# Kernel tuning notes

Measured on AMD Instinct MI355X. Metric: run time of the kernel, lower is better.

## Reference

```python
import jax, jax.numpy as jnp
import numpy as np

SEQ_LEN = 256
E = 1024      # embedding_dim (= decoder LSTM hidden size)
H = 2048      # encoder hidden_dim
LAT = 512     # latent_space_dim
CLS = 512     # common_latent_space_dim
MIX = 384     # mixture_size
VJ = 64       # embedding_dim_VJ  (constraint: 2*VJ + LAT + MIX == E)
ALPH = 32; NVG = 64; NJG = 16
X_IDX = 0; B_IDX = 1  # indices of 'X' (start) and 'B' (stop) letters


def _lstm_final(xs, h0, c0, Wih, Whh, bih, bhh):
    """Run an LSTM over xs [T, B, in] and return the final hidden state [B, H]."""
    def step(carry, x):
        h, c = carry
        g = x @ Wih.T + bih + h @ Whh.T + bhh
        i, f, gg, o = jnp.split(g, 4, axis=-1)
        c = jax.nn.sigmoid(f) * c + jax.nn.sigmoid(i) * jnp.tanh(gg)
        h = jax.nn.sigmoid(o) * jnp.tanh(c)
        return (h, c), None
    (h, c), _ = jax.lax.scan(step, (h0, c0), xs)
    return h


def _decode(h0c, Wih, Whh, bih, bhh, start_vec, end_vec, n_steps):
    """Autoregressive LSTM decode: feed previous output back as next input.
    h0c [1,E] is used as both initial h and c (as in the source)."""
    def step(carry, _):
        h, c, prev = carry
        g = prev @ Wih.T + bih + h @ Whh.T + bhh
        i, f, gg, o = jnp.split(g, 4, axis=-1)
        c2 = jax.nn.sigmoid(f) * c + jax.nn.sigmoid(i) * jnp.tanh(gg)
        h2 = jax.nn.sigmoid(o) * jnp.tanh(c2)
        return (h2, c2, h2), h2
    _, ys = jax.lax.scan(step, (h0c, h0c, start_vec), None, length=n_steps)  # [T-2,1,E]
    seq = jnp.concatenate([start_vec[None], ys, end_vec[None]], axis=0)      # [T,1,E]
    return seq[::-1]  # source reverses the list before cat


def setup_inputs() -> dict:
    key = jax.random.key(0)
    ks = jax.random.split(key, 26)
    def g(k, shape):
        return jax.random.normal(k, shape, dtype=jnp.float32) * 0.05
    return {
        "x": jax.random.randint(ks[0], (SEQ_LEN,), 0, ALPH),
        "Vg": jax.random.randint(ks[1], (1,), 0, NVG),
        "Jg": jax.random.randint(ks[2], (1,), 0, NJG),
        "emb": g(ks[3], (ALPH, E)),
        "emb_Vg": g(ks[4], (NVG, VJ)),
        "emb_Jg": g(ks[5], (NJG, VJ)),
        "enc_Wih": g(ks[6], (4 * H, E)),
        "enc_Whh": g(ks[7], (4 * H, H)),
        "enc_bih": g(ks[8], (4 * H,)),
        "enc_bhh": g(ks[9], (4 * H,)),
        "cls_W": g(ks[10], (CLS, 2 * H)), "cls_b": g(ks[11], (CLS,)),
        "latf_W": g(ks[12], (LAT, H)), "latf_b": g(ks[13], (LAT,)),
        "latr_W": g(ks[14], (LAT, H)), "latr_b": g(ks[15], (LAT,)),
        "mix_W": g(ks[16], (MIX, CLS)), "mix_b": g(ks[17], (MIX,)),
        "recf_Wih": g(ks[18], (4 * E, E)), "recf_Whh": g(ks[19], (4 * E, E)),
        "recf_bih": g(ks[20], (4 * E,)), "recf_bhh": g(ks[21], (4 * E,)),
        "recr_Wih": g(ks[22], (4 * E, E)), "recr_Whh": g(ks[23], (4 * E, E)),
        "recr_bih": g(ks[24], (4 * E,)), "recr_bhh": g(ks[25], (4 * E,)),
    }


def reference(x, Vg, Jg, emb, emb_Vg, emb_Jg,
              enc_Wih, enc_Whh, enc_bih, enc_bhh,
              cls_W, cls_b, latf_W, latf_b, latr_W, latr_b,
              mix_W, mix_b,
              recf_Wih, recf_Whh, recf_bih, recf_bhh,
              recr_Wih, recr_Whh, recr_bih, recr_bhh):
    T = x.shape[0]
    emb_f = emb[x]          # [T, E]
    emb_r = emb_f[::-1]     # reversed sequence
    h0 = jnp.zeros((1, H), jnp.float32)
    # NB: the source (bug preserved) runs the reverse pass through lstm_in_f as well.
    hf = _lstm_final(emb_f[:, None, :], h0, h0, enc_Wih, enc_Whh, enc_bih, enc_bhh)  # [1,H]
    hr = _lstm_final(emb_r[:, None, :], h0, h0, enc_Wih, enc_Whh, enc_bih, enc_bhh)  # [1,H]
    # dropout treated in eval mode (identity) for a deterministic reference
    common = jnp.tanh(jnp.concatenate([hf, hr], axis=-1) @ cls_W.T + cls_b)  # [1,CLS]
    lat_f = hf @ latf_W.T + latf_b  # [1,LAT]
    lat_r = hr @ latr_W.T + latr_b
    vg = emb_Vg[Vg]  # [1,VJ]
    jg = emb_Jg[Jg]
    lat_f_full = jnp.concatenate([vg, lat_f, jg], axis=-1)  # [1, 2*VJ+LAT]
    lat_r_full = jnp.concatenate([vg, lat_r, jg], axis=-1)
    # source (bug preserved): mixture_to_f applied to both branches
    mix = common @ mix_W.T + mix_b                      # [1,MIX]
    h0f = jnp.concatenate([lat_f_full, mix], axis=-1)   # [1,E]
    h0r = jnp.concatenate([lat_r_full, mix], axis=-1)
    start = emb[X_IDX][None]  # 'X' embedding, [1,E]
    stop = emb[B_IDX][None]   # 'B' embedding
    rec_f = _decode(h0f, recf_Wih, recf_Whh, recf_bih, recf_bhh, start, stop, T - 2)
    rec_r = _decode(h0r, recr_Wih, recr_Whh, recr_bih, recr_bhh, stop, start, T - 2)
    return (lat_f_full[None], lat_r_full[None], rec_f, rec_r, emb_f, emb_r)
```

## Files before the change

### kernel.cpp

```cpp
#include <hip/hip_runtime.h>
#include <hip/hip_fp16.h>

#define NB 256
#define NT 512


struct KArgs {
  const int *x, *Vg, *Jg;
  const float *emb, *embVg, *embJg;
  const float *encWih, *encWhh, *encBih, *encBhh;
  const float *clsW, *clsB, *latfW, *latfB, *latrW, *latrB, *mixW, *mixB;
  const float *recWih[2], *recWhh[2], *recBih[2], *recBhh[2];
  float* out;
  unsigned* barFull;
  unsigned long long *eDat, *hTdec;
  float *common, *bsum, *d1, *embf, *P;
  int fast;
};

__device__ __forceinline__ unsigned long long packtag(unsigned tag, float f) {
  return ((unsigned long long)tag << 32) | (unsigned long long)__float_as_uint(f);
}
__device__ __forceinline__ float sigm(float x) { return 1.f / (1.f + __expf(-x)); }
__device__ __forceinline__ float tanh_(float x) { return 2.f / (1.f + __expf(-2.f * x)) - 1.f; }
__device__ __forceinline__ float wred(float v) {
#pragma unroll
  for (int off = 32; off; off >>= 1) v += __shfl_xor(v, off, 64);
  return v;
}
__device__ __forceinline__ void cstoref(float* p, float v) {
  __hip_atomic_store(p, v, __ATOMIC_RELAXED, __HIP_MEMORY_SCOPE_AGENT);
}
__device__ __forceinline__ float cloadf(const float* p) {
  return __hip_atomic_load(p, __ATOMIC_RELAXED, __HIP_MEMORY_SCOPE_AGENT);
}
__device__ __forceinline__ unsigned long long cload64(const unsigned long long* p) {
  return __hip_atomic_load(p, __ATOMIC_RELAXED, __HIP_MEMORY_SCOPE_AGENT);
}
__device__ __forceinline__ void cstore64(unsigned long long* p, unsigned long long v) {
  __hip_atomic_store(p, v, __ATOMIC_RELAXED, __HIP_MEMORY_SCOPE_AGENT);
}

__device__ __forceinline__ void gbar_tree(unsigned* tree, int idx, unsigned e) {
  const int ls = 8;
  __syncthreads();
  if (threadIdx.x == 0) {
    unsigned* leaf = tree + (idx >> 3) * ls;
    unsigned* root = tree + 32 * ls;
    unsigned* flag = root + ls;
    unsigned old = __hip_atomic_fetch_add(leaf, 1u, __ATOMIC_ACQ_REL, __HIP_MEMORY_SCOPE_AGENT);
    if (old == e * 8u - 1u) {
      unsigned ro = __hip_atomic_fetch_add(root, 1u, __ATOMIC_ACQ_REL, __HIP_MEMORY_SCOPE_AGENT);
      if (ro == e * 32u - 1u)
        __hip_atomic_store(flag, e, __ATOMIC_RELEASE, __HIP_MEMORY_SCOPE_AGENT);
    }
    while (__hip_atomic_load(flag, __ATOMIC_RELAXED, __HIP_MEMORY_SCOPE_AGENT) < e)
      __builtin_amdgcn_s_sleep(2);
    __builtin_amdgcn_fence(__ATOMIC_ACQUIRE, "agent");
  }
  __syncthreads();
}

__global__ __launch_bounds__(NT, 2) void rnn2_kernel(KArgs a) {
  __shared__ float smem[16384];
  const int tid = threadIdx.x;
  const int b = blockIdx.x;
  const int wq = __builtin_amdgcn_readfirstlane(tid >> 6);
  const int lane = tid & 63;

  float* out_recf = a.out + 1280;
  float* out_recr = a.out + 1280 + 262144;
  float* out_embf = a.out + 1280 + 2 * 262144;
  float* out_embr = a.out + 1280 + 3 * 262144;

  for (int i = tid; i < 2048; i += NT) smem[i] = a.emb[i];
  __syncthreads();
  {
    int wg = b * 8 + wq;
#pragma unroll 1
    for (int rr = 0; rr < 4; rr++) {
      int idx = wg + rr * 2048;
      int dir = idx >> 12;
      int row = idx & 4095;
      const float* Wih = a.recWih[dir];
      const float* sv = &smem[dir * 1024];
      float acc = 0.f;
#pragma unroll
      for (int kc = 0; kc < 4; kc++) {
        int k = kc * 256 + lane * 4;
        float4 wv = *(const float4*)&Wih[row * 1024 + k];
        float4 ev = *(const float4*)&sv[k];
        acc += wv.x * ev.x + wv.y * ev.y + wv.z * ev.z + wv.w * ev.w;
      }
      acc = wred(acc);
      if (lane == 0)
        cstoref(&a.d1[dir * 4096 + row], acc + a.recBih[dir][row] + a.recBhh[dir][row]);
    }
  }
  const int gtid = b * NT + tid;
  const int GSZ = NB * NT;
  for (int i = gtid; i < 256 * 1024; i += GSZ) {
    int t = i >> 10, e = i & 1023;
    float v = a.emb[a.x[t] * 1024 + e];
    cstoref(&a.embf[i], v);
    out_embf[i] = v;
    out_embr[(255 - t) * 1024 + e] = v;
  }
  if (gtid < 1024) {
    int e = gtid;
    out_recf[e] = a.emb[1024 + e];
    out_recf[255 * 1024 + e] = a.emb[e];
    out_recr[e] = a.emb[e];
    out_recr[255 * 1024 + e] = a.emb[1024 + e];
  }
  if (gtid < 2048) cstore64(&a.eDat[gtid], 0ULL);
  else if (gtid < 4096) cstore64(&a.eDat[gtid], 0x0000000100000001ULL);
  if (gtid < 4096) cstore64(&a.hTdec[gtid], packtag(0xFFFFFFFFu, 0.f));
  if (gtid < 8192) {
    int dir = gtid >> 12, r = gtid & 4095;
    cstoref(&a.bsum[gtid], a.recBih[dir][r] + a.recBhh[dir][r]);
  }
  gbar_tree(a.barFull, b, 1u);

  {
    float* Pp = a.P + (size_t)b * 8192;
    const int s_td = tid >> 3;
    const int s_j = tid & 7;
#pragma unroll 1
    for (int tc = 0; tc < 4; tc++) {
      float acc[4] = {0.f, 0.f, 0.f, 0.f};
      const float* esrc = &a.embf[(size_t)(tc * 64 + s_td) * 1024];
#pragma unroll 1
      for (int kc = 0; kc < 4; kc++) {
        __syncthreads();
#pragma unroll
        for (int m = 0; m < 8; m++) {
          int kk = s_j * 32 + m * 4;
          float4 v = *(const float4*)&esrc[kc * 256 + kk];
          smem[(kk + 0) * 64 + s_td] = v.x;
          smem[(kk + 1) * 64 + s_td] = v.y;
          smem[(kk + 2) * 64 + s_td] = v.z;
          smem[(kk + 3) * 64 + s_td] = v.w;
        }
        __syncthreads();
#pragma unroll 1
        for (int k4 = 0; k4 < 64; k4++) {
          float e0 = smem[(k4 * 4 + 0) * 64 + lane];
          float e1 = smem[(k4 * 4 + 1) * 64 + lane];
          float e2 = smem[(k4 * 4 + 2) * 64 + lane];
          float e3 = smem[(k4 * 4 + 3) * 64 + lane];
#pragma unroll
          for (int g = 0; g < 4; g++) {
            const float* wp = &a.encWih[(size_t)(g * 2048 + b * 8 + wq) * 1024 + kc * 256 + k4 * 4];
            acc[g] = fmaf(e0, wp[0], fmaf(e1, wp[1], fmaf(e2, wp[2], fmaf(e3, wp[3], acc[g]))));
          }
        }
      }
#pragma unroll
      for (int g = 0; g < 4; g++) {
        int row = g * 2048 + b * 8 + wq;
        Pp[(g * 8 + wq) * 256 + tc * 64 + lane] = acc[g] + a.encBih[row] + a.encBhh[row];
      }
    }
  }
  gbar_tree(a.barFull, b, 2u);

  {
    const int u = b * 8 + wq;
    const float* Pp = a.P + (size_t)b * 8192;
    float wreg[128];
    if (a.fast) {
#pragma unroll
      for (int g = 0; g < 4; g++)
#pragma unroll
        for (int c = 0; c < 8; c++) {
          float4 wv = *(const float4*)&a.encWhh[(size_t)(g * 2048 + u) * 2048 + c * 256 + lane * 4];
          wreg[(g * 8 + c) * 4 + 0] = wv.x;
          wreg[(g * 8 + c) * 4 + 1] = wv.y;
          wreg[(g * 8 + c) * 4 + 2] = wv.z;
          wreg[(g * 8 + c) * 4 + 3] = wv.w;
        }
    }
    float cf = 0.f, cr = 0.f;
#pragma unroll 1
    for (int t = 0; t < 256; t++) {
      float pf[4], pr[4];
#pragma unroll
      for (int g = 0; g < 4; g++) {
        pf[g] = Pp[(g * 8 + wq) * 256 + t];
        pr[g] = Pp[(g * 8 + wq) * 256 + 255 - t];
      }
      {
        const unsigned long long* dp = a.eDat + (size_t)(t & 1) * 2048;
        const unsigned lo_e = (unsigned)t & 1u;
        const unsigned hi_e = ((unsigned)t >> 1) & 1u;
        unsigned long long v[4];
        for (;;) {
#pragma unroll
          for (int j = 0; j < 4; j++) v[j] = cload64(&dp[j * 512 + tid]);
          unsigned bad = 0;
#pragma unroll
          for (int j = 0; j < 4; j++)
            bad |= ((unsigned)v[j] ^ lo_e) | (((unsigned)(v[j] >> 32)) ^ hi_e);
          if (!(bad & 1u)) break;
          __builtin_amdgcn_s_sleep(1);
        }
#pragma unroll
        for (int j = 0; j < 4; j++) {
          smem[j * 512 + tid] = __uint_as_float((unsigned)v[j]);
          smem[2048 + j * 512 + tid] = __uint_as_float((unsigned)(v[j] >> 32));
        }
      }
      __syncthreads();
      float af[4] = {0, 0, 0, 0}, ar[4] = {0, 0, 0, 0};
      if (a.fast) {
#pragma unroll
        for (int c = 0; c < 8; c++) {
          float4 hf = *(const float4*)&smem[c * 256 + lane * 4];
          float4 hr = *(const float4*)&smem[2048 + c * 256 + lane * 4];
#pragma unroll
          for (int g = 0; g < 4; g++) {
            const int wb = (g * 8 + c) * 4;
            af[g] = fmaf(wreg[wb + 0], hf.x, fmaf(wreg[wb + 1], hf.y,
                    fmaf(wreg[wb + 2], hf.z, fmaf(wreg[wb + 3], hf.w, af[g]))));
            ar[g] = fmaf(wreg[wb + 0], hr.x, fmaf(wreg[wb + 1], hr.y,
                    fmaf(wreg[wb + 2], hr.z, fmaf(wreg[wb + 3], hr.w, ar[g]))));
          }
        }
      } else {
#pragma unroll 1
        for (int kc = 0; kc < 8; kc++) {
          int k = kc * 256 + lane * 4;
          float4 hf = *(const float4*)&smem[k];
          float4 hr = *(const float4*)&smem[2048 + k];
#pragma unroll
          for (int g = 0; g < 4; g++) {
            float4 wv = *(const float4*)&a.encWhh[(size_t)(g * 2048 + u) * 2048 + k];
            af[g] += wv.x * hf.x + wv.y * hf.y + wv.z * hf.z + wv.w * hf.w;
            ar[g] += wv.x * hr.x + wv.y * hr.y + wv.z * hr.z + wv.w * hr.w;
          }
        }
      }
#pragma unroll
      for (int g = 0; g < 4; g++) { af[g] = wred(af[g]); ar[g] = wred(ar[g]); }
      float gi = af[0] + pf[0], gf = af[1] + pf[1], gg = af[2] + pf[2], go = af[3] + pf[3];
      cf = sigm(gf) * cf + sigm(gi) * tanh_(gg);
      float hfv = sigm(go) * tanh_(cf);
      gi = ar[0] + pr[0]; gf = ar[1] + pr[1]; gg = ar[2] + pr[2]; go = ar[3] + pr[3];
      cr = sigm(gf) * cr + sigm(gi) * tanh_(gg);
      float hrv = sigm(go) * tanh_(cr);
      if (lane == 0) {
        unsigned tag = (unsigned)(t + 1);
        unsigned fa = (__float_as_uint(hfv) & ~1u) | (tag & 1u);
        unsigned fb = (__float_as_uint(hrv) & ~1u) | ((tag >> 1) & 1u);
        cstore64(&a.eDat[(size_t)((t + 1) & 1) * 2048 + u],
                 ((unsigned long long)fb << 32) | fa);
      }
      __syncthreads();
    }
  }

  if (b <= 192) {
    {
      const unsigned long long* dp = a.eDat;
      unsigned long long v[4];
      for (;;) {
#pragma unroll
        for (int j = 0; j < 4; j++) v[j] = cload64(&dp[j * 512 + tid]);
        unsigned bad = 0;
#pragma unroll
        for (int j = 0; j < 4; j++)
          bad |= (unsigned)v[j] | ((unsigned)(v[j] >> 32));
        if (!(bad & 1u)) break;
        __builtin_amdgcn_s_sleep(1);
      }
#pragma unroll
      for (int j = 0; j < 4; j++) {
        smem[j * 512 + tid] = __uint_as_float((unsigned)v[j]);
        smem[2048 + j * 512 + tid] = __uint_as_float((unsigned)(v[j] >> 32));
      }
    }
    __syncthreads();
    int wg = b * 8 + wq;
    if (wg < 512) {
      int r = wg;
      float acc = 0.f;
#pragma unroll 1
      for (int kc = 0; kc < 16; kc++) {
        int k = kc * 256 + lane * 4;
        float4 wv = *(const float4*)&a.clsW[(size_t)r * 4096 + k];
        float4 hv = *(const float4*)&smem[k];
        acc += wv.x * hv.x + wv.y * hv.y + wv.z * hv.z + wv.w * hv.w;
      }
      acc = wred(acc);
      if (lane == 0) cstoref(&a.common[r], tanh_(acc + a.clsB[r]));
    } else if (wg < 1024) {
      int r = wg - 512;
      float acc = 0.f;
#pragma unroll 1
      for (int kc = 0; kc < 8; kc++) {
        int k = kc * 256 + lane * 4;
        float4 wv = *(const float4*)&a.latfW[(size_t)r * 2048 + k];
        float4 hv = *(const float4*)&smem[k];
        acc += wv.x * hv.x + wv.y * hv.y + wv.z * hv.z + wv.w * hv.w;
      }
      acc = wred(acc);
      if (lane == 0) {
        float v = acc + a.latfB[r];
        cstore64(&a.hTdec[64 + r], packtag(0u, v));
        a.out[64 + r] = v;
      }
    } else if (wg < 1536) {
      int r = wg - 1024;
      float acc = 0.f;
#pragma unroll 1
      for (int kc = 0; kc < 8; kc++) {
        int k = kc * 256 + lane * 4;
        float4 wv = *(const float4*)&a.latrW[(size_t)r * 2048 + k];
        float4 hv = *(const float4*)&smem[2048 + k];
        acc += wv.x * hv.x + wv.y * hv.y + wv.z * hv.z + wv.w * hv.w;
      }
      acc = wred(acc);
      if (lane == 0) {
        float v = acc + a.latrB[r];
        cstore64(&a.hTdec[1024 + 64 + r], packtag(0u, v));
        a.out[640 + 64 + r] = v;
      }
    } else if (wg == 1536) {
      float v = a.embVg[a.Vg[0] * 64 + lane];
      cstore64(&a.hTdec[lane], packtag(0u, v));
      cstore64(&a.hTdec[1024 + lane], packtag(0u, v));
      a.out[lane] = v;
      a.out[640 + lane] = v;
    } else if (wg == 1537) {
      float v = a.embJg[a.Jg[0] * 64 + lane];
      cstore64(&a.hTdec[576 + lane], packtag(0u, v));
      cstore64(&a.hTdec[1024 + 576 + lane], packtag(0u, v));
      a.out[576 + lane] = v;
      a.out[640 + 576 + lane] = v;
    }
  }
  gbar_tree(a.barFull, b, 3u);
  if (b < 48) {
    int wg = b * 8 + wq;
    smem[tid] = cloadf(&a.common[tid]);
    __syncthreads();
    float acc = 0.f;
#pragma unroll
    for (int kc = 0; kc < 2; kc++) {
      int k = kc * 256 + lane * 4;
      float4 wv = *(const float4*)&a.mixW[(size_t)wg * 512 + k];
      float4 hv = *(const float4*)&smem[k];
      acc += wv.x * hv.x + wv.y * hv.y + wv.z * hv.z + wv.w * hv.w;
    }
    acc = wred(acc);
    if (lane == 0) {
      float v = acc + a.mixB[wg];
      cstore64(&a.hTdec[640 + wg], packtag(0u, v));
      cstore64(&a.hTdec[1024 + 640 + wg], packtag(0u, v));
    }
  }
  gbar_tree(a.barFull, b, 4u);

  {
    const int dir = b & 1;
    const int hidx = b >> 1;
    const int u = hidx * 8 + wq;
    float* outrec = dir ? out_recr : out_recf;
    float bs[4];
#pragma unroll
    for (int g = 0; g < 4; g++) bs[g] = cloadf(&a.bsum[dir * 4096 + g * 1024 + u]);
    float wd[64];
    if (a.fast) {
      const float* Wi = a.recWih[dir];
      const float* Wh = a.recWhh[dir];
#pragma unroll
      for (int g = 0; g < 4; g++)
#pragma unroll
        for (int c = 0; c < 4; c++) {
          size_t ro = (size_t)(g * 1024 + u) * 1024 + c * 256 + lane * 4;
          float4 va = *(const float4*)&Wi[ro];
          float4 vb = *(const float4*)&Wh[ro];
          wd[(g * 4 + c) * 4 + 0] = va.x + vb.x;
          wd[(g * 4 + c) * 4 + 1] = va.y + vb.y;
          wd[(g * 4 + c) * 4 + 2] = va.z + vb.z;
          wd[(g * 4 + c) * 4 + 3] = va.w + vb.w;
        }
    }
    float c = 0.f;
#pragma unroll 1
    for (int s = 1; s <= 254; s++) {
      {
        const unsigned long long* src = a.hTdec + ((s - 1) & 1) * 2048 + dir * 1024;
        const unsigned tg = (unsigned)(s - 1);
        unsigned long long v0, v1;
        for (;;) {
          v0 = cload64(&src[tid]);
          v1 = cload64(&src[512 + tid]);
          if ((((unsigned)(v0 >> 32)) ^ tg) == 0u && (((unsigned)(v1 >> 32)) ^ tg) == 0u) break;
          __builtin_amdgcn_s_sleep(1);
        }
        smem[tid] = __uint_as_float((unsigned)v0);
        smem[512 + tid] = __uint_as_float((unsigned)v1);
      }
      __syncthreads();
      float acc[4] = {0, 0, 0, 0};
      if (s == 1) {
        const float* Whh = a.recWhh[dir];
#pragma unroll 1
        for (int kc = 0; kc < 4; kc++) {
          int k = kc * 256 + lane * 4;
          float4 hv = *(const float4*)&smem[k];
#pragma unroll
          for (int g = 0; g < 4; g++) {
            float4 wv = *(const float4*)&Whh[(size_t)(g * 1024 + u) * 1024 + k];
            acc[g] += wv.x * hv.x + wv.y * hv.y + wv.z * hv.z + wv.w * hv.w;
          }
        }
      } else if (a.fast) {
#pragma unroll
        for (int cc = 0; cc < 4; cc++) {
          float4 hv = *(const float4*)&smem[cc * 256 + lane * 4];
#pragma unroll
          for (int g = 0; g < 4; g++) {
            const int wb = (g * 4 + cc) * 4;
            acc[g] = fmaf(wd[wb + 0], hv.x, fmaf(wd[wb + 1], hv.y,
                     fmaf(wd[wb + 2], hv.z, fmaf(wd[wb + 3], hv.w, acc[g]))));
          }
        }
      } else {
        const float* Wi = a.recWih[dir];
        const float* Wh = a.recWhh[dir];
#pragma unroll 1
        for (int kc = 0; kc < 4; kc++) {
          int k = kc * 256 + lane * 4;
          float4 hv = *(const float4*)&smem[k];
#pragma unroll
          for (int g = 0; g < 4; g++) {
            size_t ro = (size_t)(g * 1024 + u) * 1024 + k;
            float4 va = *(const float4*)&Wi[ro];
            float4 vb = *(const float4*)&Wh[ro];
            acc[g] += (va.x + vb.x) * hv.x + (va.y + vb.y) * hv.y +
                      (va.z + vb.z) * hv.z + (va.w + vb.w) * hv.w;
          }
        }
      }
#pragma unroll
      for (int g = 0; g < 4; g++) acc[g] = wred(acc[g]);
      float gi, gf, gg, go;
      if (s == 1) {
        gi = acc[0] + cloadf(&a.d1[dir * 4096 + u]);
        gf = acc[1] + cloadf(&a.d1[dir * 4096 + 1024 + u]);
        gg = acc[2] + cloadf(&a.d1[dir * 4096 + 2048 + u]);
        go = acc[3] + cloadf(&a.d1[dir * 4096 + 3072 + u]);
        c = smem[u];
      } else {
        gi = acc[0] + bs[0]; gf = acc[1] + bs[1]; gg = acc[2] + bs[2]; go = acc[3] + bs[3];
      }
      c = sigm(gf) * c + sigm(gi) * tanh_(gg);
      float h2 = sigm(go) * tanh_(c);
      if (lane == 0) {
        outrec[(size_t)(255 - s) * 1024 + u] = h2;
        if (s < 254)
          cstore64(&a.hTdec[(s & 1) * 2048 + dir * 1024 + u], packtag((unsigned)s, h2));
      }
      __syncthreads();
    }
  }
}

extern "C" void kernel_launch(void* const* d_in, const int* in_sizes, int n_in,
                              void* d_out, int out_size, void* d_ws, size_t ws_size,
                              hipStream_t stream) {
  (void)in_sizes; (void)n_in; (void)out_size;
  KArgs a;
  a.x = (const int*)d_in[0];
  a.Vg = (const int*)d_in[1];
  a.Jg = (const int*)d_in[2];
  a.emb = (const float*)d_in[3];
  a.embVg = (const float*)d_in[4];
  a.embJg = (const float*)d_in[5];
  a.encWih = (const float*)d_in[6];
  a.encWhh = (const float*)d_in[7];
  a.encBih = (const float*)d_in[8];
  a.encBhh = (const float*)d_in[9];
  a.clsW = (const float*)d_in[10];
  a.clsB = (const float*)d_in[11];
  a.latfW = (const float*)d_in[12];
  a.latfB = (const float*)d_in[13];
  a.latrW = (const float*)d_in[14];
  a.latrB = (const float*)d_in[15];
  a.mixW = (const float*)d_in[16];
  a.mixB = (const float*)d_in[17];
  a.recWih[0] = (const float*)d_in[18];
  a.recWhh[0] = (const float*)d_in[19];
  a.recBih[0] = (const float*)d_in[20];
  a.recBhh[0] = (const float*)d_in[21];
  a.recWih[1] = (const float*)d_in[22];
  a.recWhh[1] = (const float*)d_in[23];
  a.recBih[1] = (const float*)d_in[24];
  a.recBhh[1] = (const float*)d_in[25];
  a.out = (float*)d_out;
  char* ws = (char*)d_ws;
  a.barFull = (unsigned*)ws;
  a.eDat = (unsigned long long*)(ws + 4096);
  a.hTdec = (unsigned long long*)(ws + 36864);
  a.common = (float*)(ws + 69632);
  a.bsum = (float*)(ws + 71680);
  a.d1 = (float*)(ws + 104448);
  a.embf = (float*)(ws + 137216);
  a.P = (float*)(ws + 1204224);
  a.fast = (ws_size >= 9592832ULL) ? 1 : 0;
  hipMemsetAsync(ws, 0, 4096, stream);
  hipLaunchKernelGGL(rnn2_kernel, dim3(NB), dim3(NT), 0, stream, a);
}
```

Baseline: 2.010 ms.

## Swizzle LDS transpose, skip step-zero poll, use lighter barriers in recurrences

XOR-swizzles the shared-memory column index in the input-projection transpose to avoid bank conflicts on writes. Skips the global poll at encoder step zero by zeroing the hidden state directly. Replaces the trailing __syncthreads in the encoder and decoder recurrent loops with a raw s_barrier plus compiler memory fences, dropping the waitcnt/fence overhead. The lighter barrier relies on ordering the compiler and hardware may not guarantee, which risks races on LDS reuse.

After: 2.032 ms. Within noise of the previous version (+1.1%).

```diff
diff --git a/kernel.cpp b/kernel.cpp
--- a/kernel.cpp
+++ b/kernel.cpp
@@ -1,5 +1,4 @@
 #include <hip/hip_runtime.h>
-#include <hip/hip_fp16.h>
 
 #define NB 256
 #define NT 512
@@ -28,6 +27,11 @@
   for (int off = 32; off; off >>= 1) v += __shfl_xor(v, off, 64);
   return v;
 }
+__device__ __forceinline__ void softbar() {
+  asm volatile("" ::: "memory");
+  __builtin_amdgcn_s_barrier();
+  asm volatile("" ::: "memory");
+}
 __device__ __forceinline__ void cstoref(float* p, float v) {
   __hip_atomic_store(p, v, __ATOMIC_RELAXED, __HIP_MEMORY_SCOPE_AGENT);
 }
@@ -136,19 +140,21 @@
 #pragma unroll
         for (int m = 0; m < 8; m++) {
           int kk = s_j * 32 + m * 4;
+          int col = s_td ^ ((kk >> 2) & 63);
           float4 v = *(const float4*)&esrc[kc * 256 + kk];
-          smem[(kk + 0) * 64 + s_td] = v.x;
-          smem[(kk + 1) * 64 + s_td] = v.y;
-          smem[(kk + 2) * 64 + s_td] = v.z;
-          smem[(kk + 3) * 64 + s_td] = v.w;
+          smem[(kk + 0) * 64 + col] = v.x;
+          smem[(kk + 1) * 64 + col] = v.y;
+          smem[(kk + 2) * 64 + col] = v.z;
+          smem[(kk + 3) * 64 + col] = v.w;
         }
         __syncthreads();
 #pragma unroll 1
         for (int k4 = 0; k4 < 64; k4++) {
-          float e0 = smem[(k4 * 4 + 0) * 64 + lane];
-          float e1 = smem[(k4 * 4 + 1) * 64 + lane];
-          float e2 = smem[(k4 * 4 + 2) * 64 + lane];
-          float e3 = smem[(k4 * 4 + 3) * 64 + lane];
+          int cw = lane ^ k4;
+          float e0 = smem[(k4 * 4 + 0) * 64 + cw];
+          float e1 = smem[(k4 * 4 + 1) * 64 + cw];
+          float e2 = smem[(k4 * 4 + 2) * 64 + cw];
+          float e3 = smem[(k4 * 4 + 3) * 64 + cw];
 #pragma unroll
           for (int g = 0; g < 4; g++) {
             const float* wp = &a.encWih[(size_t)(g * 2048 + b * 8 + wq) * 1024 + kc * 256 + k4 * 4];
@@ -195,20 +201,25 @@
         const unsigned lo_e = (unsigned)t & 1u;
         const unsigned hi_e = ((unsigned)t >> 1) & 1u;
         unsigned long long v[4];
-        for (;;) {
-#pragma unroll
-          for (int j = 0; j < 4; j++) v[j] = cload64(&dp[j * 512 + tid]);
-          unsigned bad = 0;
-#pragma unroll
-          for (int j = 0; j < 4; j++)
-            bad |= ((unsigned)v[j] ^ lo_e) | (((unsigned)(v[j] >> 32)) ^ hi_e);
-          if (!(bad & 1u)) break;
-          __builtin_amdgcn_s_sleep(1);
-        }
-#pragma unroll
-        for (int j = 0; j < 4; j++) {
-          smem[j * 512 + tid] = __uint_as_float((unsigned)v[j]);
-          smem[2048 + j * 512 + tid] = __uint_as_float((unsigned)(v[j] >> 32));
+        if (t == 0) {
+#pragma unroll
+          for (int j = 0; j < 8; j++) smem[j * 512 + tid] = 0.f;
+        } else {
+          for (;;) {
+#pragma unroll
+            for (int j = 0; j < 4; j++) v[j] = cload64(&dp[j * 512 + tid]);
+            unsigned bad = 0;
+#pragma unroll
+            for (int j = 0; j < 4; j++)
+              bad |= ((unsigned)v[j] ^ lo_e) | (((unsigned)(v[j] >> 32)) ^ hi_e);
+            if (!(bad & 1u)) break;
+            __builtin_amdgcn_s_sleep(1);
+          }
+#pragma unroll
+          for (int j = 0; j < 4; j++) {
+            smem[j * 512 + tid] = __uint_as_float((unsigned)v[j]);
+            smem[2048 + j * 512 + tid] = __uint_as_float((unsigned)(v[j] >> 32));
+          }
         }
       }
       __syncthreads();
@@ -256,7 +267,7 @@
         cstore64(&a.eDat[(size_t)((t + 1) & 1) * 2048 + u],
                  ((unsigned long long)fb << 32) | fa);
       }
-      __syncthreads();
+      softbar();
     }
   }
 
@@ -464,7 +475,7 @@
         if (s < 254)
           cstore64(&a.hTdec[(s & 1) * 2048 + dir * 1024 + u], packtag((unsigned)s, h2));
       }
-      __syncthreads();
+      softbar();
     }
   }
 }
```
